# Optimization experiments

Hardware: AMD Instinct MI355X
Metric: run time of the kernel (lower is better)

The kernel has to match this reference:

```python
import jax, jax.numpy as jnp
import numpy as np

D_MODEL, D_K, D_V, H = 1024, 64, 64, 16
B, NQ, NK = 8, 1024, 1024


def setup_inputs() -> dict:
    key = jax.random.key(0)
    ks = jax.random.split(key, 12)
    s = 0.02
    queries = jax.random.normal(ks[0], (B, NQ, D_MODEL), jnp.float32)
    keys_ = jax.random.normal(ks[1], (B, NK, D_MODEL), jnp.float32)
    values = jax.random.normal(ks[2], (B, NK, D_MODEL), jnp.float32)
    attention_weights = jax.random.uniform(ks[3], (B, H, NQ, NK), jnp.float32)
    # causal mask: True = masked; strict upper triangle so no row is fully masked
    attention_mask = ~jnp.tril(jnp.ones((NQ, NK), dtype=bool))[None, None]
    Wq = jax.random.normal(ks[4], (H * D_K, D_MODEL), jnp.float32) * s
    Wk = jax.random.normal(ks[5], (H * D_K, D_MODEL), jnp.float32) * s
    Wv = jax.random.normal(ks[6], (H * D_V, D_MODEL), jnp.float32) * s
    Wo = jax.random.normal(ks[7], (D_MODEL, H * D_V), jnp.float32) * s
    bq = jnp.zeros((H * D_K,), jnp.float32)
    bk = jnp.zeros((H * D_K,), jnp.float32)
    bv = jnp.zeros((H * D_V,), jnp.float32)
    bo = jnp.zeros((D_MODEL,), jnp.float32)
    return dict(queries=queries, keys=keys_, values=values,
                attention_weights=attention_weights, attention_mask=attention_mask,
                Wq=Wq, bq=bq, Wk=Wk, bk=bk, Wv=Wv, bv=bv, Wo=Wo, bo=bo)


def reference(queries, keys, values, attention_weights, attention_mask,
              Wq, bq, Wk, bk, Wv, bv, Wo, bo):
    b_s, nq, _ = queries.shape
    nk = keys.shape[1]
    # torch Linear: y = x @ W.T + b
    q = (queries @ Wq.T + bq).reshape(b_s, nq, H, D_K).transpose(0, 2, 1, 3)  # b h q d
    k = (keys @ Wk.T + bk).reshape(b_s, nk, H, D_K).transpose(0, 2, 1, 3)     # b h k d
    v = (values @ Wv.T + bv).reshape(b_s, nk, H, D_V).transpose(0, 2, 1, 3)   # b h k d
    att = jnp.einsum('bhqd,bhkd->bhqk', q, k) / np.sqrt(D_K).astype(np.float32)
    att = att * attention_weights
    att = jnp.where(attention_mask, -jnp.inf, att)
    att = jax.nn.softmax(att, axis=-1)
    out = jnp.einsum('bhqk,bhkd->bqhd', att, v).reshape(b_s, nq, H * D_V)
    return out @ Wo.T + bo
```

## Files before the change

kernel.cpp:

```cpp
#include <hip/hip_runtime.h>
#include <hip/hip_bf16.h>


typedef unsigned short u16;
typedef __attribute__((ext_vector_type(8))) short short8;
typedef __attribute__((ext_vector_type(4))) float float4v;

__device__ __forceinline__ u16 f2bf(float f) {
    unsigned int u = __float_as_uint(f);
    u = (u + 0x7fffu + ((u >> 16) & 1u)) >> 16;
    return (u16)u;
}

template <bool OUT_BF16>
__global__ __launch_bounds__(256) void proj_gemm(const float* __restrict__ A,
                                                 const float* __restrict__ W,
                                                 const float* __restrict__ bias,
                                                 void* __restrict__ C) {
    __shared__ __align__(16) u16 As[128][72];
    __shared__ __align__(16) u16 Bs[128][72];

    const int tid  = threadIdx.x;
    const int m0   = blockIdx.x * 128, n0 = blockIdx.y * 128;
    const int lane = tid & 63, w = tid >> 6;
    const int wm   = (w & 1) * 64, wn = (w >> 1) * 64;
    const int c    = lane & 15, quad = lane >> 4;

    const int lr = tid >> 4;
    const int lc = (tid & 15) * 4;

    float4v acc[4][4] = {};

    for (int kb = 0; kb < 1024; kb += 64) {
#pragma unroll
        for (int i = 0; i < 8; ++i) {
            int row = lr + i * 16;
            float4 va = *(const float4*)&A[(size_t)(m0 + row) * 1024 + kb + lc];
            float4 vb = *(const float4*)&W[(size_t)(n0 + row) * 1024 + kb + lc];
            As[row][lc + 0] = f2bf(va.x); As[row][lc + 1] = f2bf(va.y);
            As[row][lc + 2] = f2bf(va.z); As[row][lc + 3] = f2bf(va.w);
            Bs[row][lc + 0] = f2bf(vb.x); Bs[row][lc + 1] = f2bf(vb.y);
            Bs[row][lc + 2] = f2bf(vb.z); Bs[row][lc + 3] = f2bf(vb.w);
        }
        __syncthreads();
#pragma unroll
        for (int ks = 0; ks < 2; ++ks) {
            short8 a[4], b[4];
#pragma unroll
            for (int i = 0; i < 4; ++i)
                a[i] = *(const short8*)&As[wm + i * 16 + c][ks * 32 + quad * 8];
#pragma unroll
            for (int i = 0; i < 4; ++i)
                b[i] = *(const short8*)&Bs[wn + i * 16 + c][ks * 32 + quad * 8];
#pragma unroll
            for (int i = 0; i < 4; ++i)
#pragma unroll
                for (int j = 0; j < 4; ++j)
                    acc[i][j] = __builtin_amdgcn_mfma_f32_16x16x32_bf16(a[i], b[j], acc[i][j], 0, 0, 0);
        }
        __syncthreads();
    }

#pragma unroll
    for (int j = 0; j < 4; ++j) {
        int n = n0 + wn + j * 16 + c;
        float bv = bias[n];
#pragma unroll
        for (int i = 0; i < 4; ++i) {
            int mb = m0 + wm + i * 16 + quad * 4;
#pragma unroll
            for (int r = 0; r < 4; ++r) {
                float v = acc[i][j][r] + bv;
                size_t off = (size_t)(mb + r) * 1024 + n;
                if (OUT_BF16) ((u16*)C)[off] = f2bf(v);
                else          ((float*)C)[off] = v;
            }
        }
    }
}

__global__ __launch_bounds__(256) void transpose_v(const u16* __restrict__ Vb,
                                                   u16* __restrict__ Vt) {
    __shared__ __align__(16) u16 t[64][72];
    const int bh = blockIdx.y, b = bh >> 4, h = bh & 15;
    const int k0 = blockIdx.x * 64;
    const int tid = threadIdx.x;
    {
        int key = tid >> 2, d0 = (tid & 3) << 4;
        const uint4* src = (const uint4*)&Vb[(size_t)(b * 1024 + k0 + key) * 1024 + h * 64 + d0];
        *(uint4*)&t[key][d0]     = src[0];
        *(uint4*)&t[key][d0 + 8] = src[1];
    }
    __syncthreads();
    {
        int d = tid & 63, kg = (tid >> 6) << 4;
        uint4 o[2];
        u16* op = (u16*)o;
#pragma unroll
        for (int i = 0; i < 16; ++i) op[i] = t[kg + i][d];
        uint4* dst = (uint4*)&Vt[((size_t)bh * 64 + d) * 1024 + k0 + kg];
        dst[0] = o[0];
        dst[1] = o[1];
    }
}

__global__ __launch_bounds__(256) void attn_kernel(const u16* __restrict__ Qb,
                                                   const u16* __restrict__ Kb,
                                                   const u16* __restrict__ Vt,
                                                   const float* __restrict__ Wts,
                                                   float* __restrict__ AO) {
    __shared__ __align__(16) u16 Plds[4][16][72];

    const int qt = blockIdx.x;
    const int bh = blockIdx.y;
    const int b  = bh >> 4, h = bh & 15;
    const int q0 = qt * 64;
    const int tid = threadIdx.x, lane = tid & 63, w = tid >> 6;
    const int c = lane & 15, quad = lane >> 4;
    const int qrow = q0 + w * 16;

    short8 qf[2];
#pragma unroll
    for (int ks = 0; ks < 2; ++ks)
        qf[ks] = *(const short8*)&Qb[(size_t)(b * 1024 + qrow + c) * 1024 + h * 64 + ks * 32 + quad * 8];

    float m_run[4], l_run[4];
    float4v o[4] = {};
#pragma unroll
    for (int r = 0; r < 4; ++r) { m_run[r] = -1e30f; l_run[r] = 0.f; }

    for (int kt = 0; kt <= qt; ++kt) {
        const int k0 = kt * 64;
        float4v s[4] = {};
#pragma unroll
        for (int ks = 0; ks < 2; ++ks) {
#pragma unroll
            for (int t = 0; t < 4; ++t) {
                short8 kf = *(const short8*)&Kb[(size_t)(b * 1024 + k0 + t * 16 + c) * 1024 + h * 64 + ks * 32 + quad * 8];
                s[t] = __builtin_amdgcn_mfma_f32_16x16x32_bf16(qf[ks], kf, s[t], 0, 0, 0);
            }
        }
        const bool diag = (kt == qt);
        const float* wp = &Wts[((size_t)bh * 1024 + (qrow + quad * 4)) * 1024 + k0 + c];
#pragma unroll
        for (int t = 0; t < 4; ++t)
#pragma unroll
            for (int r = 0; r < 4; ++r) {
                float wv = wp[(size_t)r * 1024 + t * 16];
                float v = s[t][r] * 0.125f * wv;
                if (diag && (k0 + t * 16 + c) > (qrow + quad * 4 + r)) v = -1e30f;
                s[t][r] = v;
            }
        float alpha[4];
#pragma unroll
        for (int r = 0; r < 4; ++r) {
            float v = fmaxf(fmaxf(s[0][r], s[1][r]), fmaxf(s[2][r], s[3][r]));
#pragma unroll
            for (int off = 1; off < 16; off <<= 1) v = fmaxf(v, __shfl_xor(v, off, 64));
            float mn = fmaxf(m_run[r], v);
            alpha[r] = __expf(m_run[r] - mn);
            m_run[r] = mn;
        }
#pragma unroll
        for (int r = 0; r < 4; ++r) {
            float sum = 0.f;
#pragma unroll
            for (int t = 0; t < 4; ++t) {
                float p = __expf(s[t][r] - m_run[r]);
                s[t][r] = p;
                sum += p;
            }
#pragma unroll
            for (int off = 1; off < 16; off <<= 1) sum += __shfl_xor(sum, off, 64);
            l_run[r] = l_run[r] * alpha[r] + sum;
        }
#pragma unroll
        for (int t = 0; t < 4; ++t)
#pragma unroll
            for (int r = 0; r < 4; ++r)
                Plds[w][quad * 4 + r][t * 16 + c] = f2bf(s[t][r]);
        __syncthreads();
#pragma unroll
        for (int dt = 0; dt < 4; ++dt)
#pragma unroll
            for (int r = 0; r < 4; ++r) o[dt][r] *= alpha[r];
#pragma unroll
        for (int ks = 0; ks < 2; ++ks) {
            short8 pf = *(const short8*)&Plds[w][c][ks * 32 + quad * 8];
#pragma unroll
            for (int dt = 0; dt < 4; ++dt) {
                short8 vf = *(const short8*)&Vt[((size_t)bh * 64 + dt * 16 + c) * 1024 + k0 + ks * 32 + quad * 8];
                o[dt] = __builtin_amdgcn_mfma_f32_16x16x32_bf16(pf, vf, o[dt], 0, 0, 0);
            }
        }
        __syncthreads();
    }
#pragma unroll
    for (int dt = 0; dt < 4; ++dt)
#pragma unroll
        for (int r = 0; r < 4; ++r) {
            float v = o[dt][r] / l_run[r];
            AO[(size_t)(b * 1024 + qrow + quad * 4 + r) * 1024 + h * 64 + dt * 16 + c] = v;
        }
}

extern "C" void kernel_launch(void* const* d_in, const int* in_sizes, int n_in,
                              void* d_out, int out_size, void* d_ws, size_t ws_size,
                              hipStream_t stream) {
    const float* q   = (const float*)d_in[0];
    const float* k   = (const float*)d_in[1];
    const float* v   = (const float*)d_in[2];
    const float* aw  = (const float*)d_in[3];
    const float* Wq  = (const float*)d_in[5];
    const float* bq  = (const float*)d_in[6];
    const float* Wk  = (const float*)d_in[7];
    const float* bk  = (const float*)d_in[8];
    const float* Wv  = (const float*)d_in[9];
    const float* bv  = (const float*)d_in[10];
    const float* Wo  = (const float*)d_in[11];
    const float* bo  = (const float*)d_in[12];

    u16*   Qb = (u16*)d_ws;
    u16*   Kb = Qb + 8388608;
    u16*   Vb = Kb + 8388608;
    u16*   Vt = Vb + 8388608;
    float* AO = (float*)(Vt + 8388608);

    dim3 blk(256), pg(64, 8);
    proj_gemm<true><<<pg, blk, 0, stream>>>(q, Wq, bq, Qb);
    proj_gemm<true><<<pg, blk, 0, stream>>>(k, Wk, bk, Kb);
    proj_gemm<true><<<pg, blk, 0, stream>>>(v, Wv, bv, Vb);
    transpose_v<<<dim3(16, 128), blk, 0, stream>>>(Vb, Vt);
    attn_kernel<<<dim3(16, 128), blk, 0, stream>>>(Qb, Kb, Vt, aw, AO);
    proj_gemm<false><<<pg, blk, 0, stream>>>(AO, Wo, bo, (float*)d_out);
}
```

Measured before the change: 1.095 ms.

## Pre-convert inputs to bf16, stage tiles via global_load_lds, batch QKV GEMMs

Adds a bulk fp32-to-bf16 conversion kernel for activations and weights, so the GEMMs load bf16 tiles straight into LDS with global_load_lds instead of converting per tile. The three QKV projections are merged into one launch using blockIdx.z. The attention kernel now stages K and V tiles in LDS, issues the attention-weight loads before the sync, drops one barrier, and writes its output as bf16 for the final projection. This trades an extra conversion pass and more workspace for less per-tile conversion work and fewer redundant global reads. The unpadded 64-wide LDS rows may cause bank conflicts.

```diff
diff --git a/kernel.cpp b/kernel.cpp
--- a/kernel.cpp
+++ b/kernel.cpp
@@ -1,5 +1,4 @@
 #include <hip/hip_runtime.h>
-#include <hip/hip_bf16.h>
 
 
 typedef unsigned short u16;
@@ -12,35 +11,65 @@
     return (u16)u;
 }
 
+__device__ __forceinline__ void glds16(const void* g, void* l) {
+    __builtin_amdgcn_global_load_lds(
+        (const __attribute__((address_space(1))) unsigned int*)g,
+        (__attribute__((address_space(3))) unsigned int*)l, 16, 0, 0);
+}
+
+__global__ __launch_bounds__(256) void convert_bf16(const float* s0, const float* s1,
+                                                    const float* s2, const float* s3,
+                                                    const float* s4, const float* s5,
+                                                    const float* s6, u16* base) {
+    const size_t offs[7] = {0, 8388608, 16777216, 25165824, 26214400, 27262976, 28311552};
+    const int    ns[7]   = {8388608, 8388608, 8388608, 1048576, 1048576, 1048576, 1048576};
+    const float* srcs[7] = {s0, s1, s2, s3, s4, s5, s6};
+    const int t = blockIdx.y;
+    const float* src = srcs[t];
+    u16* dst = base + offs[t];
+    const int n8 = ns[t] >> 3;
+    const int stride = gridDim.x * 256;
+    for (int i = blockIdx.x * 256 + threadIdx.x; i < n8; i += stride) {
+        float4 a = ((const float4*)src)[i * 2];
+        float4 b = ((const float4*)src)[i * 2 + 1];
+        uint4 o;
+        o.x = (unsigned)f2bf(a.x) | ((unsigned)f2bf(a.y) << 16);
+        o.y = (unsigned)f2bf(a.z) | ((unsigned)f2bf(a.w) << 16);
+        o.z = (unsigned)f2bf(b.x) | ((unsigned)f2bf(b.y) << 16);
+        o.w = (unsigned)f2bf(b.z) | ((unsigned)f2bf(b.w) << 16);
+        ((uint4*)dst)[i] = o;
+    }
+}
+
 template <bool OUT_BF16>
-__global__ __launch_bounds__(256) void proj_gemm(const float* __restrict__ A,
-                                                 const float* __restrict__ W,
-                                                 const float* __restrict__ bias,
-                                                 void* __restrict__ C) {
-    __shared__ __align__(16) u16 As[128][72];
-    __shared__ __align__(16) u16 Bs[128][72];
-
-    const int tid  = threadIdx.x;
-    const int m0   = blockIdx.x * 128, n0 = blockIdx.y * 128;
-    const int lane = tid & 63, w = tid >> 6;
-    const int wm   = (w & 1) * 64, wn = (w >> 1) * 64;
-    const int c    = lane & 15, quad = lane >> 4;
-
-    const int lr = tid >> 4;
-    const int lc = (tid & 15) * 4;
+__global__ __launch_bounds__(256) void gemm_bt(const u16* __restrict__ Ab,
+                                               const u16* __restrict__ Wb,
+                                               const float* b0, const float* b1,
+                                               const float* b2, void* Cb,
+                                               size_t Astride, size_t Wstride,
+                                               size_t Cstride) {
+    __shared__ __align__(16) u16 As[8192];
+    __shared__ __align__(16) u16 Bs[8192];
+
+    const int z = blockIdx.z;
+    const u16* A = Ab + (size_t)z * Astride;
+    const u16* W = Wb + (size_t)z * Wstride;
+    const float* bias = (z == 0) ? b0 : (z == 1) ? b1 : b2;
+
+    const int m0 = blockIdx.x * 128, n0 = blockIdx.y * 128;
+    const int tid = threadIdx.x, lane = tid & 63, w = tid >> 6;
+    const int wm = (w & 1) * 64, wn = (w >> 1) * 64;
+    const int c = lane & 15, quad = lane >> 4;
+    const int srow = tid >> 3;
+    const int scol = (tid & 7) * 8;
 
     float4v acc[4][4] = {};
 
     for (int kb = 0; kb < 1024; kb += 64) {
 #pragma unroll
-        for (int i = 0; i < 8; ++i) {
-            int row = lr + i * 16;
-            float4 va = *(const float4*)&A[(size_t)(m0 + row) * 1024 + kb + lc];
-            float4 vb = *(const float4*)&W[(size_t)(n0 + row) * 1024 + kb + lc];
-            As[row][lc + 0] = f2bf(va.x); As[row][lc + 1] = f2bf(va.y);
-            As[row][lc + 2] = f2bf(va.z); As[row][lc + 3] = f2bf(va.w);
-            Bs[row][lc + 0] = f2bf(vb.x); Bs[row][lc + 1] = f2bf(vb.y);
-            Bs[row][lc + 2] = f2bf(vb.z); Bs[row][lc + 3] = f2bf(vb.w);
+        for (int i = 0; i < 4; ++i) {
+            glds16(&A[(size_t)(m0 + i * 32 + srow) * 1024 + kb + scol], &As[i * 2048 + w * 512]);
+            glds16(&W[(size_t)(n0 + i * 32 + srow) * 1024 + kb + scol], &Bs[i * 2048 + w * 512]);
         }
         __syncthreads();
 #pragma unroll
@@ -48,10 +77,10 @@
             short8 a[4], b[4];
 #pragma unroll
             for (int i = 0; i < 4; ++i)
-                a[i] = *(const short8*)&As[wm + i * 16 + c][ks * 32 + quad * 8];
-#pragma unroll
-            for (int i = 0; i < 4; ++i)
-                b[i] = *(const short8*)&Bs[wn + i * 16 + c][ks * 32 + quad * 8];
+                a[i] = *(const short8*)&As[(wm + i * 16 + c) * 64 + ks * 32 + quad * 8];
+#pragma unroll
+            for (int j = 0; j < 4; ++j)
+                b[j] = *(const short8*)&Bs[(wn + j * 16 + c) * 64 + ks * 32 + quad * 8];
 #pragma unroll
             for (int i = 0; i < 4; ++i)
 #pragma unroll
@@ -72,8 +101,8 @@
             for (int r = 0; r < 4; ++r) {
                 float v = acc[i][j][r] + bv;
                 size_t off = (size_t)(mb + r) * 1024 + n;
-                if (OUT_BF16) ((u16*)C)[off] = f2bf(v);
-                else          ((float*)C)[off] = v;
+                if (OUT_BF16) ((u16*)Cb + (size_t)z * Cstride)[off] = f2bf(v);
+                else          ((float*)Cb)[off] = v;
             }
         }
     }
@@ -108,16 +137,19 @@
                                                    const u16* __restrict__ Kb,
                                                    const u16* __restrict__ Vt,
                                                    const float* __restrict__ Wts,
-                                                   float* __restrict__ AO) {
-    __shared__ __align__(16) u16 Plds[4][16][72];
+                                                   u16* __restrict__ AO) {
+    __shared__ __align__(16) u16 Ks[4096];
+    __shared__ __align__(16) u16 Vs[4096];
+    __shared__ __align__(16) u16 Pl[4][1024];
 
     const int qt = blockIdx.x;
     const int bh = blockIdx.y;
-    const int b  = bh >> 4, h = bh & 15;
+    const int b = bh >> 4, h = bh & 15;
     const int q0 = qt * 64;
     const int tid = threadIdx.x, lane = tid & 63, w = tid >> 6;
     const int c = lane & 15, quad = lane >> 4;
     const int qrow = q0 + w * 16;
+    const int srow = tid >> 3, scol = (tid & 7) * 8;
 
     short8 qf[2];
 #pragma unroll
@@ -131,23 +163,34 @@
 
     for (int kt = 0; kt <= qt; ++kt) {
         const int k0 = kt * 64;
+#pragma unroll
+        for (int i = 0; i < 2; ++i) {
+            glds16(&Kb[(size_t)(b * 1024 + k0 + i * 32 + srow) * 1024 + h * 64 + scol],
+                   &Ks[i * 2048 + w * 512]);
+            glds16(&Vt[((size_t)bh * 64 + i * 32 + srow) * 1024 + k0 + scol],
+                   &Vs[i * 2048 + w * 512]);
+        }
+        float wv[4][4];
+        const float* wp = &Wts[((size_t)bh * 1024 + (qrow + quad * 4)) * 1024 + k0 + c];
+#pragma unroll
+        for (int t = 0; t < 4; ++t)
+#pragma unroll
+            for (int r = 0; r < 4; ++r) wv[t][r] = wp[(size_t)r * 1024 + t * 16];
+        __syncthreads();
         float4v s[4] = {};
 #pragma unroll
-        for (int ks = 0; ks < 2; ++ks) {
+        for (int ks = 0; ks < 2; ++ks)
 #pragma unroll
             for (int t = 0; t < 4; ++t) {
-                short8 kf = *(const short8*)&Kb[(size_t)(b * 1024 + k0 + t * 16 + c) * 1024 + h * 64 + ks * 32 + quad * 8];
+                short8 kf = *(const short8*)&Ks[(t * 16 + c) * 64 + ks * 32 + quad * 8];
                 s[t] = __builtin_amdgcn_mfma_f32_16x16x32_bf16(qf[ks], kf, s[t], 0, 0, 0);
             }
-        }
         const bool diag = (kt == qt);
-        const float* wp = &Wts[((size_t)bh * 1024 + (qrow + quad * 4)) * 1024 + k0 + c];
 #pragma unroll
         for (int t = 0; t < 4; ++t)
 #pragma unroll
             for (int r = 0; r < 4; ++r) {
-                float wv = wp[(size_t)r * 1024 + t * 16];
-                float v = s[t][r] * 0.125f * wv;
+                float v = s[t][r] * 0.125f * wv[t][r];
                 if (diag && (k0 + t * 16 + c) > (qrow + quad * 4 + r)) v = -1e30f;
                 s[t][r] = v;
             }
@@ -178,18 +221,17 @@
         for (int t = 0; t < 4; ++t)
 #pragma unroll
             for (int r = 0; r < 4; ++r)
-                Plds[w][quad * 4 + r][t * 16 + c] = f2bf(s[t][r]);
-        __syncthreads();
+                Pl[w][(quad * 4 + r) * 64 + t * 16 + c] = f2bf(s[t][r]);
 #pragma unroll
         for (int dt = 0; dt < 4; ++dt)
 #pragma unroll
             for (int r = 0; r < 4; ++r) o[dt][r] *= alpha[r];
 #pragma unroll
         for (int ks = 0; ks < 2; ++ks) {
-            short8 pf = *(const short8*)&Plds[w][c][ks * 32 + quad * 8];
+            short8 pf = *(const short8*)&Pl[w][c * 64 + ks * 32 + quad * 8];
 #pragma unroll
             for (int dt = 0; dt < 4; ++dt) {
-                short8 vf = *(const short8*)&Vt[((size_t)bh * 64 + dt * 16 + c) * 1024 + k0 + ks * 32 + quad * 8];
+                short8 vf = *(const short8*)&Vs[(dt * 16 + c) * 64 + ks * 32 + quad * 8];
                 o[dt] = __builtin_amdgcn_mfma_f32_16x16x32_bf16(pf, vf, o[dt], 0, 0, 0);
             }
         }
@@ -198,39 +240,43 @@
 #pragma unroll
     for (int dt = 0; dt < 4; ++dt)
 #pragma unroll
-        for (int r = 0; r < 4; ++r) {
-            float v = o[dt][r] / l_run[r];
-            AO[(size_t)(b * 1024 + qrow + quad * 4 + r) * 1024 + h * 64 + dt * 16 + c] = v;
-        }
+        for (int r = 0; r < 4; ++r)
+            AO[(size_t)(b * 1024 + qrow + quad * 4 + r) * 1024 + h * 64 + dt * 16 + c] =
+                f2bf(o[dt][r] / l_run[r]);
 }
 
 extern "C" void kernel_launch(void* const* d_in, const int* in_sizes, int n_in,
                               void* d_out, int out_size, void* d_ws, size_t ws_size,
                               hipStream_t stream) {
-    const float* q   = (const float*)d_in[0];
-    const float* k   = (const float*)d_in[1];
-    const float* v   = (const float*)d_in[2];
-    const float* aw  = (const float*)d_in[3];
-    const float* Wq  = (const float*)d_in[5];
-    const float* bq  = (const float*)d_in[6];
-    const float* Wk  = (const float*)d_in[7];
-    const float* bk  = (const float*)d_in[8];
-    const float* Wv  = (const float*)d_in[9];
-    const float* bv  = (const float*)d_in[10];
-    const float* Wo  = (const float*)d_in[11];
-    const float* bo  = (const float*)d_in[12];
-
-    u16*   Qb = (u16*)d_ws;
-    u16*   Kb = Qb + 8388608;
-    u16*   Vb = Kb + 8388608;
-    u16*   Vt = Vb + 8388608;
-    float* AO = (float*)(Vt + 8388608);
-
-    dim3 blk(256), pg(64, 8);
-    proj_gemm<true><<<pg, blk, 0, stream>>>(q, Wq, bq, Qb);
-    proj_gemm<true><<<pg, blk, 0, stream>>>(k, Wk, bk, Kb);
-    proj_gemm<true><<<pg, blk, 0, stream>>>(v, Wv, bv, Vb);
+    const float* q  = (const float*)d_in[0];
+    const float* k  = (const float*)d_in[1];
+    const float* v  = (const float*)d_in[2];
+    const float* aw = (const float*)d_in[3];
+    const float* bq = (const float*)d_in[6];
+    const float* bk = (const float*)d_in[8];
+    const float* bv = (const float*)d_in[10];
+    const float* Wo = (const float*)d_in[11];
+    const float* bo = (const float*)d_in[12];
+    const float* Wq = (const float*)d_in[5];
+    const float* Wk = (const float*)d_in[7];
+    const float* Wv = (const float*)d_in[9];
+
+    u16* ws16 = (u16*)d_ws;
+    u16* qkvbf = ws16;
+    u16* Wbf   = ws16 + 25165824;
+    u16* Wob   = ws16 + 28311552;
+    u16* Qb    = ws16 + 29360128;
+    u16* Kb    = Qb + 8388608;
+    u16* Vb    = Kb + 8388608;
+    u16* Vt    = Vb + 8388608;
+    u16* AObf  = Vt + 8388608;
+
+    dim3 blk(256);
+    convert_bf16<<<dim3(512, 7), blk, 0, stream>>>(q, k, v, Wq, Wk, Wv, Wo, ws16);
+    gemm_bt<true><<<dim3(64, 8, 3), blk, 0, stream>>>(qkvbf, Wbf, bq, bk, bv, Qb,
+                                                      8388608, 1048576, 8388608);
     transpose_v<<<dim3(16, 128), blk, 0, stream>>>(Vb, Vt);
-    attn_kernel<<<dim3(16, 128), blk, 0, stream>>>(Qb, Kb, Vt, aw, AO);
-    proj_gemm<false><<<pg, blk, 0, stream>>>(AO, Wo, bo, (float*)d_out);
-}
+    attn_kernel<<<dim3(16, 128), blk, 0, stream>>>(Qb, Kb, Vt, aw, AObf);
+    gemm_bt<false><<<dim3(64, 8, 1), blk, 0, stream>>>(AObf, Wob, bo, bo, bo, d_out,
+                                                       0, 0, 0);
+}
```

Measured after the change: 955.5 us. 12.7% less time.
